# Kernel optimization log

Measured on AMD Instinct MI355X. Metric: run time of the kernel, lower is better.

The kernel has to match this reference:

```python
import jax, jax.numpy as jnp
import numpy as np

B, S, E = 16, 1024, 512
D = 2 * E            # dim of concatenated embeddings, input to QKV and MLP
H1, H2 = 2048, 1024  # hidden_dims
SCALE = float(1.0 / np.sqrt(E))  # code scales by embedding_dim**0.5 (the init arg, not D)


def setup_inputs() -> dict:
    key = jax.random.key(0)
    k = jax.random.split(key, 12)

    def lin_w(kk, fan_in, fan_out):
        return jax.random.normal(kk, (fan_in, fan_out), jnp.float32) * float(1.0 / np.sqrt(fan_in))

    return {
        "emb1": jax.random.normal(k[0], (B, S, E), jnp.float32),
        "emb2": jax.random.normal(k[1], (B, S, E), jnp.float32),
        # query-row masks; all ones (a 0 would -inf an entire softmax row -> NaN)
        "mask1": jnp.ones((B, S // 2), jnp.int32),
        "mask2": jnp.ones((B, S // 2), jnp.int32),
        "Wq": lin_w(k[2], D, D), "bq": jnp.zeros((D,), jnp.float32),
        "Wk": lin_w(k[3], D, D), "bk": jnp.zeros((D,), jnp.float32),
        "Wv": lin_w(k[4], D, D), "bv": jnp.zeros((D,), jnp.float32),
        "W1": lin_w(k[5], D, H1), "b1": jnp.zeros((H1,), jnp.float32),
        "W2": lin_w(k[6], H1, H2), "b2": jnp.zeros((H2,), jnp.float32),
        "W3": lin_w(k[7], H2, 1), "b3": jnp.zeros((1,), jnp.float32),
    }


def reference(emb1, emb2, mask1, mask2, Wq, bq, Wk, bk, Wv, bv, W1, b1, W2, b2, W3, b3):
    x = jnp.concatenate([emb1, emb2], axis=-1)        # [B, S, D]
    mask = jnp.concatenate([mask1, mask2], axis=-1)   # [B, S] (query-row mask)

    # QKV self-attention with query-only mask
    Q = x @ Wq + bq
    K = x @ Wk + bk
    V = x @ Wv + bv
    scores = jnp.einsum("bqd,bkd->bqk", Q, K) * SCALE  # [B, S, S]
    scores = jnp.where(mask[:, :, None] == 0, -jnp.inf, scores)
    attn = jax.nn.softmax(scores, axis=-1)
    attended = jnp.einsum("bqk,bkd->bqd", attn, V)     # [B, S, D]

    # MLP head (Dropout is identity in eval mode)
    h = jax.nn.relu(attended @ W1 + b1)
    h = jax.nn.relu(h @ W2 + b2)
    logits = h @ W3 + b3                               # [B, S, 1]
    return jax.nn.sigmoid(logits)
```

## Files before the change

### kernel.cpp

```cpp
#include <hip/hip_runtime.h>
#include <math.h>

#define DEV __device__ __forceinline__

typedef unsigned short u16;
typedef unsigned int   u32;
typedef __bf16 bf16x8 __attribute__((ext_vector_type(8)));
typedef float  f32x4  __attribute__((ext_vector_type(4)));
typedef u16    u16x8  __attribute__((ext_vector_type(8)));
typedef u16    u16x4  __attribute__((ext_vector_type(4)));

DEV u16 f2b(float f) {
  u32 u = __builtin_bit_cast(u32, f);
  u = (u + 0x7FFFu + ((u >> 16) & 1u)) >> 16;
  return (u16)u;
}
DEV float b2f(u16 h) { u32 u = (u32)h << 16; return __builtin_bit_cast(float, u); }

DEV void gl_lds16(const u16* g, u16* l) {
  __builtin_amdgcn_global_load_lds((const __attribute__((address_space(1))) void*)g,
                                   (__attribute__((address_space(3))) void*)l, 16, 0, 0);
}

DEV float wred_max(float v) {
#pragma unroll
  for (int o = 32; o > 0; o >>= 1) v = fmaxf(v, __shfl_xor(v, o, 64));
  return v;
}
DEV float wred_sum(float v) {
#pragma unroll
  for (int o = 32; o > 0; o >>= 1) v += __shfl_xor(v, o, 64);
  return v;
}

__global__ __launch_bounds__(256) void concat_convert(
    const float* __restrict__ e1, const float* __restrict__ e2, u16* __restrict__ xb) {
  const size_t idx = ((size_t)blockIdx.x * 256 + threadIdx.x) * 8;
  const int d = (int)(idx & 1023);
  const size_t row = idx >> 10;
  const float* s = (d < 512) ? (e1 + row * 512 + d) : (e2 + row * 512 + (d - 512));
  f32x4 a = *(const f32x4*)s;
  f32x4 b = *(const f32x4*)(s + 4);
  u16x8 o;
  o[0]=f2b(a[0]); o[1]=f2b(a[1]); o[2]=f2b(a[2]); o[3]=f2b(a[3]);
  o[4]=f2b(b[0]); o[5]=f2b(b[1]); o[6]=f2b(b[2]); o[7]=f2b(b[3]);
  *(u16x8*)(xb + idx) = o;
}

__global__ __launch_bounds__(256) void transpose_w(
    const float* __restrict__ W, int ldi, u16* __restrict__ WT, int ldo) {
  __shared__ float tile[64][65];
  const int tx = threadIdx.x & 63, ty = threadIdx.x >> 6;
  const int r0 = blockIdx.y * 64, c0 = blockIdx.x * 64;
#pragma unroll
  for (int i = 0; i < 16; ++i)
    tile[ty + 4*i][tx] = W[(size_t)(r0 + ty + 4*i) * ldi + c0 + tx];
  __syncthreads();
#pragma unroll
  for (int i = 0; i < 16; ++i)
    WT[(size_t)(c0 + ty + 4*i) * ldo + r0 + tx] = f2b(tile[tx][ty + 4*i]);
}

__global__ void concat_bias(const float* __restrict__ bq, const float* __restrict__ bk,
                            float* __restrict__ o) {
  int i = blockIdx.x * 256 + threadIdx.x;
  o[i] = (i < 1024) ? bq[i] : bk[i - 1024];
}

template<int F32OUT, int RELU, int RBIAS>
__global__ __launch_bounds__(512, 2) void gemm256(
    const u16* __restrict__ A, int lda, long long sA,
    const u16* __restrict__ B, int ldb, long long sB,
    void* __restrict__ C, int ldc, long long sC,
    const float* __restrict__ bias, float scale, int K) {
  __shared__ __align__(16) u16 lds[4][2][8192];

  const int t  = threadIdx.x;
  const int ln = t & 63, wv = t >> 6;

  int bx, by, bz;
  {
    const int gx = gridDim.x, gy = gridDim.y, gz = gridDim.z;
    const int nwg = gx * gy * gz;
    const int F = (blockIdx.z * gy + blockIdx.y) * gx + blockIdx.x;
    const int q = nwg >> 3;
    const int L = (F & 7) * q + (F >> 3);
    if (gz > 1) {
      const int pb = gx * gy;
      bz = L / pb; const int r = L - bz * pb;
      by = r / gx; bx = r - by * gx;
    } else {
      bz = 0;
      const int sh = ((gy & 7) == 0) ? 8 : 4;
      const int sw = gx * sh;
      const int sy = L / sw; const int r = L - sy * sw;
      bx = r / sh; by = sy * sh + (r - bx * sh);
    }
  }
  const int m0 = by * 256, n0 = bx * 256;
  A += (size_t)bz * (size_t)sA; B += (size_t)bz * (size_t)sB;

  const int srow = t >> 2;
  const int sgr  = (t & 3) ^ ((t >> 3) & 3);
  const u16* gA = A + (size_t)(m0 + srow) * lda + sgr * 8;
  const u16* gB = B + (size_t)(n0 + srow) * ldb + sgr * 8;
  const size_t a128 = (size_t)128 * lda, b128 = (size_t)128 * ldb;
  const int ldst = wv * 512;

  const int l15 = ln & 15, lhi = ln >> 4;
  const int wm = (wv >> 2) * 128, wn = (wv & 3) * 64;

  int offA[8], offB[4];
#pragma unroll
  for (int i = 0; i < 8; ++i) {
    const int r = wm + i * 16 + l15;
    offA[i] = r * 32 + ((lhi ^ ((r >> 1) & 3)) << 3);
  }
#pragma unroll
  for (int j = 0; j < 4; ++j) {
    const int r = wn + j * 16 + l15;
    offB[j] = r * 32 + ((lhi ^ ((r >> 1) & 3)) << 3);
  }

  f32x4 acc[8][4] = {};
  const int KT = K >> 5;

#pragma unroll
  for (int pt = 0; pt < 3; ++pt) {
    const u16* _ga = gA + (size_t)pt * 32;
    const u16* _gb = gB + (size_t)pt * 32;
    u16* _la = &lds[pt][0][ldst];
    u16* _lb = &lds[pt][1][ldst];
    gl_lds16(_ga, _la); gl_lds16(_ga + a128, _la + 4096);
    gl_lds16(_gb, _lb); gl_lds16(_gb + b128, _lb + 4096);
  }
  asm volatile("s_waitcnt vmcnt(8)" ::: "memory");
  __builtin_amdgcn_sched_barrier(0);
  __builtin_amdgcn_s_barrier();

  for (int kt = 0; kt < KT; ++kt) {
    const u16* Abuf = &lds[kt & 3][0][0];
    const u16* Bbuf = &lds[kt & 3][1][0];
    const int  nt   = kt + 3;

    bf16x8 a0 = *(const bf16x8*)&Abuf[offA[0]];
    bf16x8 a1 = *(const bf16x8*)&Abuf[offA[1]];
    bf16x8 a2 = *(const bf16x8*)&Abuf[offA[2]];
    bf16x8 a3 = *(const bf16x8*)&Abuf[offA[3]];
    bf16x8 b0 = *(const bf16x8*)&Bbuf[offB[0]];
    bf16x8 b1 = *(const bf16x8*)&Bbuf[offB[1]];
    bf16x8 b2 = *(const bf16x8*)&Bbuf[offB[2]];
    bf16x8 b3 = *(const bf16x8*)&Bbuf[offB[3]];
    if (nt < KT) {
      const u16* _ga = gA + (size_t)nt * 32;
      u16* _la = &lds[nt & 3][0][ldst];
      gl_lds16(_ga, _la); gl_lds16(_ga + a128, _la + 4096);
    }
    __builtin_amdgcn_s_barrier();
    __builtin_amdgcn_s_setprio(1);
    acc[0][0] = __builtin_amdgcn_mfma_f32_16x16x32_bf16(a0, b0, acc[0][0], 0, 0, 0);
    acc[0][1] = __builtin_amdgcn_mfma_f32_16x16x32_bf16(a0, b1, acc[0][1], 0, 0, 0);
    acc[0][2] = __builtin_amdgcn_mfma_f32_16x16x32_bf16(a0, b2, acc[0][2], 0, 0, 0);
    acc[0][3] = __builtin_amdgcn_mfma_f32_16x16x32_bf16(a0, b3, acc[0][3], 0, 0, 0);
    acc[1][0] = __builtin_amdgcn_mfma_f32_16x16x32_bf16(a1, b0, acc[1][0], 0, 0, 0);
    acc[1][1] = __builtin_amdgcn_mfma_f32_16x16x32_bf16(a1, b1, acc[1][1], 0, 0, 0);
    acc[1][2] = __builtin_amdgcn_mfma_f32_16x16x32_bf16(a1, b2, acc[1][2], 0, 0, 0);
    acc[1][3] = __builtin_amdgcn_mfma_f32_16x16x32_bf16(a1, b3, acc[1][3], 0, 0, 0);
    acc[2][0] = __builtin_amdgcn_mfma_f32_16x16x32_bf16(a2, b0, acc[2][0], 0, 0, 0);
    acc[2][1] = __builtin_amdgcn_mfma_f32_16x16x32_bf16(a2, b1, acc[2][1], 0, 0, 0);
    acc[2][2] = __builtin_amdgcn_mfma_f32_16x16x32_bf16(a2, b2, acc[2][2], 0, 0, 0);
    acc[2][3] = __builtin_amdgcn_mfma_f32_16x16x32_bf16(a2, b3, acc[2][3], 0, 0, 0);
    acc[3][0] = __builtin_amdgcn_mfma_f32_16x16x32_bf16(a3, b0, acc[3][0], 0, 0, 0);
    acc[3][1] = __builtin_amdgcn_mfma_f32_16x16x32_bf16(a3, b1, acc[3][1], 0, 0, 0);
    acc[3][2] = __builtin_amdgcn_mfma_f32_16x16x32_bf16(a3, b2, acc[3][2], 0, 0, 0);
    acc[3][3] = __builtin_amdgcn_mfma_f32_16x16x32_bf16(a3, b3, acc[3][3], 0, 0, 0);
    __builtin_amdgcn_s_setprio(0);
    __builtin_amdgcn_s_barrier();

    bf16x8 a4 = *(const bf16x8*)&Abuf[offA[4]];
    bf16x8 a5 = *(const bf16x8*)&Abuf[offA[5]];
    bf16x8 a6 = *(const bf16x8*)&Abuf[offA[6]];
    bf16x8 a7 = *(const bf16x8*)&Abuf[offA[7]];
    if (nt < KT) {
      const u16* _gb = gB + (size_t)nt * 32;
      u16* _lb = &lds[nt & 3][1][ldst];
      gl_lds16(_gb, _lb); gl_lds16(_gb + b128, _lb + 4096);
    }
    __builtin_amdgcn_s_barrier();
    __builtin_amdgcn_s_setprio(1);
    acc[4][0] = __builtin_amdgcn_mfma_f32_16x16x32_bf16(a4, b0, acc[4][0], 0, 0, 0);
    acc[4][1] = __builtin_amdgcn_mfma_f32_16x16x32_bf16(a4, b1, acc[4][1], 0, 0, 0);
    acc[4][2] = __builtin_amdgcn_mfma_f32_16x16x32_bf16(a4, b2, acc[4][2], 0, 0, 0);
    acc[4][3] = __builtin_amdgcn_mfma_f32_16x16x32_bf16(a4, b3, acc[4][3], 0, 0, 0);
    acc[5][0] = __builtin_amdgcn_mfma_f32_16x16x32_bf16(a5, b0, acc[5][0], 0, 0, 0);
    acc[5][1] = __builtin_amdgcn_mfma_f32_16x16x32_bf16(a5, b1, acc[5][1], 0, 0, 0);
    acc[5][2] = __builtin_amdgcn_mfma_f32_16x16x32_bf16(a5, b2, acc[5][2], 0, 0, 0);
    acc[5][3] = __builtin_amdgcn_mfma_f32_16x16x32_bf16(a5, b3, acc[5][3], 0, 0, 0);
    acc[6][0] = __builtin_amdgcn_mfma_f32_16x16x32_bf16(a6, b0, acc[6][0], 0, 0, 0);
    acc[6][1] = __builtin_amdgcn_mfma_f32_16x16x32_bf16(a6, b1, acc[6][1], 0, 0, 0);
    acc[6][2] = __builtin_amdgcn_mfma_f32_16x16x32_bf16(a6, b2, acc[6][2], 0, 0, 0);
    acc[6][3] = __builtin_amdgcn_mfma_f32_16x16x32_bf16(a6, b3, acc[6][3], 0, 0, 0);
    acc[7][0] = __builtin_amdgcn_mfma_f32_16x16x32_bf16(a7, b0, acc[7][0], 0, 0, 0);
    acc[7][1] = __builtin_amdgcn_mfma_f32_16x16x32_bf16(a7, b1, acc[7][1], 0, 0, 0);
    acc[7][2] = __builtin_amdgcn_mfma_f32_16x16x32_bf16(a7, b2, acc[7][2], 0, 0, 0);
    acc[7][3] = __builtin_amdgcn_mfma_f32_16x16x32_bf16(a7, b3, acc[7][3], 0, 0, 0);
    __builtin_amdgcn_s_setprio(0);

    if (kt < KT - 3)       { asm volatile("s_waitcnt vmcnt(8)" ::: "memory"); }
    else if (kt == KT - 3) { asm volatile("s_waitcnt vmcnt(4)" ::: "memory"); }
    else if (kt == KT - 2) { asm volatile("s_waitcnt vmcnt(0)" ::: "memory"); }
    __builtin_amdgcn_sched_barrier(0);
    __builtin_amdgcn_s_barrier();
  }

  const size_t cb = (size_t)bz * (size_t)sC;
#pragma unroll
  for (int i = 0; i < 8; ++i) {
    const int rg = m0 + wm + i * 16 + lhi * 4;
#pragma unroll
    for (int j = 0; j < 4; ++j) {
      const int cg = n0 + wn + j * 16 + l15;
      const float cbv = (!RBIAS && bias) ? bias[cg] : 0.f;
#pragma unroll
      for (int r = 0; r < 4; ++r) {
        float v = acc[i][j][r] * scale + (RBIAS ? bias[rg + r] : cbv);
        if (RELU) v = fmaxf(v, 0.f);
        if (F32OUT) ((float*)C)[cb + (size_t)(rg + r) * ldc + cg] = v;
        else        ((u16*)C)[cb + (size_t)(rg + r) * ldc + cg] = f2b(v);
      }
    }
  }
}

__global__ __launch_bounds__(256) void softmax_mask(
    const float* __restrict__ sc, const int* __restrict__ m1,
    const int* __restrict__ m2, u16* __restrict__ attn) {
  __shared__ float red[8];
  const int row = blockIdx.x;
  const int b = row >> 10, q = row & 1023;
  const int mk = (q < 512) ? m1[b * 512 + q] : m2[b * 512 + q - 512];
  f32x4 v = ((const f32x4*)(sc + (size_t)row * 1024))[threadIdx.x];
  if (mk == 0) { v[0] = v[1] = v[2] = v[3] = -INFINITY; }
  float mx = fmaxf(fmaxf(v[0], v[1]), fmaxf(v[2], v[3]));
  mx = wred_max(mx);
  const int ln = threadIdx.x & 63, wv = threadIdx.x >> 6;
  if (ln == 0) red[wv] = mx;
  __syncthreads();
  mx = fmaxf(fmaxf(red[0], red[1]), fmaxf(red[2], red[3]));
  float e0 = __expf(v[0] - mx), e1 = __expf(v[1] - mx);
  float e2 = __expf(v[2] - mx), e3 = __expf(v[3] - mx);
  float s = wred_sum(e0 + e1 + e2 + e3);
  if (ln == 0) red[4 + wv] = s;
  __syncthreads();
  const float inv = 1.f / (red[4] + red[5] + red[6] + red[7]);
  u16x4 o; o[0] = f2b(e0 * inv); o[1] = f2b(e1 * inv); o[2] = f2b(e2 * inv); o[3] = f2b(e3 * inv);
  *(u16x4*)(attn + (size_t)row * 1024 + threadIdx.x * 4) = o;
}

__global__ __launch_bounds__(256) void logits_sigmoid(
    const u16* __restrict__ h2, const float* __restrict__ W3,
    const float* __restrict__ b3, float* __restrict__ out) {
  const int wid = (blockIdx.x * 256 + threadIdx.x) >> 6;
  const int ln = threadIdx.x & 63;
  const u16* r = h2 + (size_t)wid * 1024 + ln * 16;
  u16x8 v0 = *(const u16x8*)r;
  u16x8 v1 = *(const u16x8*)(r + 8);
  const float* w = W3 + ln * 16;
  float s = 0.f;
#pragma unroll
  for (int i = 0; i < 8; ++i) s += b2f(v0[i]) * w[i];
#pragma unroll
  for (int i = 0; i < 8; ++i) s += b2f(v1[i]) * w[8 + i];
#pragma unroll
  for (int o = 32; o > 0; o >>= 1) s += __shfl_down(s, o, 64);
  if (ln == 0) out[wid] = 1.f / (1.f + __expf(-(s + b3[0])));
}

extern "C" void kernel_launch(void* const* d_in, const int* in_sizes, int n_in,
                              void* d_out, int out_size, void* d_ws, size_t ws_size,
                              hipStream_t stream) {
  (void)in_sizes; (void)n_in; (void)out_size; (void)ws_size;
  const float* emb1 = (const float*)d_in[0];
  const float* emb2 = (const float*)d_in[1];
  const int*   mask1 = (const int*)d_in[2];
  const int*   mask2 = (const int*)d_in[3];
  const float* Wq = (const float*)d_in[4];  const float* bq = (const float*)d_in[5];
  const float* Wk = (const float*)d_in[6];  const float* bk = (const float*)d_in[7];
  const float* Wv = (const float*)d_in[8];  const float* bv = (const float*)d_in[9];
  const float* W1 = (const float*)d_in[10]; const float* b1 = (const float*)d_in[11];
  const float* W2 = (const float*)d_in[12]; const float* b2 = (const float*)d_in[13];
  const float* W3 = (const float*)d_in[14]; const float* b3 = (const float*)d_in[15];

  char* ws = (char*)d_ws;
  u16*  XB    = (u16*)(ws + 0);
  u16*  QK    = (u16*)(ws + 33554432);
  u16*  VT    = (u16*)(ws + 100663296);
  float* SC   = (float*)(ws + 134217728);
  u16*  WTQKV = (u16*)(ws + 201326592);
  u16*  W1T   = (u16*)(ws + 207618048);
  u16*  W2T   = (u16*)(ws + 211812352);
  float* BF_  = (float*)(ws + 216006656);
  u16*  ATTN  = XB;
  u16*  ATT   = (u16*)(ws + 134217728);
  u16*  H1    = QK;
  u16*  H2    = VT;
  float* out  = (float*)d_out;

  const float SCALE = 0.04419417382415922f;

  concat_convert<<<8192, 256, 0, stream>>>(emb1, emb2, XB);
  transpose_w<<<dim3(16, 16), 256, 0, stream>>>(Wq, 1024, WTQKV, 1024);
  transpose_w<<<dim3(16, 16), 256, 0, stream>>>(Wk, 1024, WTQKV + 1024 * 1024, 1024);
  transpose_w<<<dim3(16, 16), 256, 0, stream>>>(Wv, 1024, WTQKV + 2048 * 1024, 1024);
  transpose_w<<<dim3(32, 16), 256, 0, stream>>>(W1, 2048, W1T, 1024);
  transpose_w<<<dim3(16, 32), 256, 0, stream>>>(W2, 1024, W2T, 2048);
  concat_bias<<<8, 256, 0, stream>>>(bq, bk, BF_);

  gemm256<0, 0, 0><<<dim3(8, 64, 1), 512, 0, stream>>>(
      XB, 1024, 0, WTQKV, 1024, 0, QK, 2048, 0, BF_, 1.f, 1024);
  gemm256<0, 0, 1><<<dim3(64, 4, 1), 512, 0, stream>>>(
      WTQKV + 2048 * 1024, 1024, 0, XB, 1024, 0, VT, 16384, 0, bv, 1.f, 1024);
  gemm256<1, 0, 0><<<dim3(4, 4, 16), 512, 0, stream>>>(
      QK, 2048, 2097152LL, QK + 1024, 2048, 2097152LL,
      SC, 1024, 1048576LL, nullptr, SCALE, 1024);
  softmax_mask<<<16384, 256, 0, stream>>>(SC, mask1, mask2, ATTN);
  gemm256<0, 0, 0><<<dim3(4, 4, 16), 512, 0, stream>>>(
      ATTN, 1024, 1048576LL, VT, 16384, 1024LL,
      ATT, 1024, 1048576LL, nullptr, 1.f, 1024);
  gemm256<0, 1, 0><<<dim3(8, 64, 1), 512, 0, stream>>>(
      ATT, 1024, 0, W1T, 1024, 0, H1, 2048, 0, b1, 1.f, 1024);
  gemm256<0, 1, 0><<<dim3(4, 64, 1), 512, 0, stream>>>(
      H1, 2048, 0, W2T, 2048, 0, H2, 1024, 0, b2, 1.f, 2048);
  logits_sigmoid<<<4096, 256, 0, stream>>>(H2, W3, b3, out);
}
```

Baseline: 414.0 us.

## Software-pipeline LDS fragment loads across k-iterations in the GEMM main loop

Restructures the GEMM k-loop so the A/B fragments for the next k-tile are read from LDS while the current tile's second-half MFMAs execute. Global-to-LDS staging for a tile is issued as a single block at the top of each iteration, and barriers drop from four to two per iteration, with manual lgkmcnt waits to order LDS reads against MFMAs. This aims to hide LDS read latency and barrier stalls behind matrix-core work. In exchange it raises register pressure from the extra live fragment registers, and the hand-set wait counts must match exactly for the kernel to stay correct.

```diff
diff --git a/kernel.cpp b/kernel.cpp
--- a/kernel.cpp
+++ b/kernel.cpp
@@ -2,6 +2,7 @@
 #include <math.h>
 
 #define DEV __device__ __forceinline__
+#define SB0() __builtin_amdgcn_sched_barrier(0)
 
 typedef unsigned short u16;
 typedef unsigned int   u32;
@@ -125,93 +126,91 @@
   f32x4 acc[8][4] = {};
   const int KT = K >> 5;
 
-#pragma unroll
-  for (int pt = 0; pt < 3; ++pt) {
-    const u16* _ga = gA + (size_t)pt * 32;
-    const u16* _gb = gB + (size_t)pt * 32;
-    u16* _la = &lds[pt][0][ldst];
-    u16* _lb = &lds[pt][1][ldst];
-    gl_lds16(_ga, _la); gl_lds16(_ga + a128, _la + 4096);
-    gl_lds16(_gb, _lb); gl_lds16(_gb + b128, _lb + 4096);
-  }
+#define STAGE(tile)                                                       \
+  {                                                                       \
+    const int rb = (tile) & 3;                                            \
+    const u16* _ga = gA + (size_t)(tile) * 32;                            \
+    const u16* _gb = gB + (size_t)(tile) * 32;                            \
+    u16* _la = &lds[rb][0][ldst];                                         \
+    u16* _lb = &lds[rb][1][ldst];                                         \
+    gl_lds16(_ga, _la); gl_lds16(_ga + a128, _la + 4096);                 \
+    gl_lds16(_gb, _lb); gl_lds16(_gb + b128, _lb + 4096);                 \
+  }
+#define MF(i, j, Av, Bv) \
+  acc[i][j] = __builtin_amdgcn_mfma_f32_16x16x32_bf16(Av, Bv, acc[i][j], 0, 0, 0)
+
+  STAGE(0); STAGE(1); STAGE(2);
   asm volatile("s_waitcnt vmcnt(8)" ::: "memory");
-  __builtin_amdgcn_sched_barrier(0);
+  SB0();
   __builtin_amdgcn_s_barrier();
+  bf16x8 pa0, pa1, pa2, pa3, pb0, pb1, pb2, pb3;
+  {
+    const u16* Ab = &lds[0][0][0];
+    const u16* Bb = &lds[0][1][0];
+    pb0 = *(const bf16x8*)&Bb[offB[0]]; pb1 = *(const bf16x8*)&Bb[offB[1]];
+    pb2 = *(const bf16x8*)&Bb[offB[2]]; pb3 = *(const bf16x8*)&Bb[offB[3]];
+    pa0 = *(const bf16x8*)&Ab[offA[0]]; pa1 = *(const bf16x8*)&Ab[offA[1]];
+    pa2 = *(const bf16x8*)&Ab[offA[2]]; pa3 = *(const bf16x8*)&Ab[offA[3]];
+  }
 
   for (int kt = 0; kt < KT; ++kt) {
-    const u16* Abuf = &lds[kt & 3][0][0];
-    const u16* Bbuf = &lds[kt & 3][1][0];
-    const int  nt   = kt + 3;
-
-    bf16x8 a0 = *(const bf16x8*)&Abuf[offA[0]];
-    bf16x8 a1 = *(const bf16x8*)&Abuf[offA[1]];
-    bf16x8 a2 = *(const bf16x8*)&Abuf[offA[2]];
-    bf16x8 a3 = *(const bf16x8*)&Abuf[offA[3]];
-    bf16x8 b0 = *(const bf16x8*)&Bbuf[offB[0]];
-    bf16x8 b1 = *(const bf16x8*)&Bbuf[offB[1]];
-    bf16x8 b2 = *(const bf16x8*)&Bbuf[offB[2]];
-    bf16x8 b3 = *(const bf16x8*)&Bbuf[offB[3]];
-    if (nt < KT) {
-      const u16* _ga = gA + (size_t)nt * 32;
-      u16* _la = &lds[nt & 3][0][ldst];
-      gl_lds16(_ga, _la); gl_lds16(_ga + a128, _la + 4096);
-    }
-    __builtin_amdgcn_s_barrier();
-    __builtin_amdgcn_s_setprio(1);
-    acc[0][0] = __builtin_amdgcn_mfma_f32_16x16x32_bf16(a0, b0, acc[0][0], 0, 0, 0);
-    acc[0][1] = __builtin_amdgcn_mfma_f32_16x16x32_bf16(a0, b1, acc[0][1], 0, 0, 0);
-    acc[0][2] = __builtin_amdgcn_mfma_f32_16x16x32_bf16(a0, b2, acc[0][2], 0, 0, 0);
-    acc[0][3] = __builtin_amdgcn_mfma_f32_16x16x32_bf16(a0, b3, acc[0][3], 0, 0, 0);
-    acc[1][0] = __builtin_amdgcn_mfma_f32_16x16x32_bf16(a1, b0, acc[1][0], 0, 0, 0);
-    acc[1][1] = __builtin_amdgcn_mfma_f32_16x16x32_bf16(a1, b1, acc[1][1], 0, 0, 0);
-    acc[1][2] = __builtin_amdgcn_mfma_f32_16x16x32_bf16(a1, b2, acc[1][2], 0, 0, 0);
-    acc[1][3] = __builtin_amdgcn_mfma_f32_16x16x32_bf16(a1, b3, acc[1][3], 0, 0, 0);
-    acc[2][0] = __builtin_amdgcn_mfma_f32_16x16x32_bf16(a2, b0, acc[2][0], 0, 0, 0);
-    acc[2][1] = __builtin_amdgcn_mfma_f32_16x16x32_bf16(a2, b1, acc[2][1], 0, 0, 0);
-    acc[2][2] = __builtin_amdgcn_mfma_f32_16x16x32_bf16(a2, b2, acc[2][2], 0, 0, 0);
-    acc[2][3] = __builtin_amdgcn_mfma_f32_16x16x32_bf16(a2, b3, acc[2][3], 0, 0, 0);
-    acc[3][0] = __builtin_amdgcn_mfma_f32_16x16x32_bf16(a3, b0, acc[3][0], 0, 0, 0);
-    acc[3][1] = __builtin_amdgcn_mfma_f32_16x16x32_bf16(a3, b1, acc[3][1], 0, 0, 0);
-    acc[3][2] = __builtin_amdgcn_mfma_f32_16x16x32_bf16(a3, b2, acc[3][2], 0, 0, 0);
-    acc[3][3] = __builtin_amdgcn_mfma_f32_16x16x32_bf16(a3, b3, acc[3][3], 0, 0, 0);
-    __builtin_amdgcn_s_setprio(0);
-    __builtin_amdgcn_s_barrier();
-
-    bf16x8 a4 = *(const bf16x8*)&Abuf[offA[4]];
-    bf16x8 a5 = *(const bf16x8*)&Abuf[offA[5]];
-    bf16x8 a6 = *(const bf16x8*)&Abuf[offA[6]];
-    bf16x8 a7 = *(const bf16x8*)&Abuf[offA[7]];
-    if (nt < KT) {
-      const u16* _gb = gB + (size_t)nt * 32;
-      u16* _lb = &lds[nt & 3][1][ldst];
-      gl_lds16(_gb, _lb); gl_lds16(_gb + b128, _lb + 4096);
-    }
-    __builtin_amdgcn_s_barrier();
-    __builtin_amdgcn_s_setprio(1);
-    acc[4][0] = __builtin_amdgcn_mfma_f32_16x16x32_bf16(a4, b0, acc[4][0], 0, 0, 0);
-    acc[4][1] = __builtin_amdgcn_mfma_f32_16x16x32_bf16(a4, b1, acc[4][1], 0, 0, 0);
-    acc[4][2] = __builtin_amdgcn_mfma_f32_16x16x32_bf16(a4, b2, acc[4][2], 0, 0, 0);
-    acc[4][3] = __builtin_amdgcn_mfma_f32_16x16x32_bf16(a4, b3, acc[4][3], 0, 0, 0);
-    acc[5][0] = __builtin_amdgcn_mfma_f32_16x16x32_bf16(a5, b0, acc[5][0], 0, 0, 0);
-    acc[5][1] = __builtin_amdgcn_mfma_f32_16x16x32_bf16(a5, b1, acc[5][1], 0, 0, 0);
-    acc[5][2] = __builtin_amdgcn_mfma_f32_16x16x32_bf16(a5, b2, acc[5][2], 0, 0, 0);
-    acc[5][3] = __builtin_amdgcn_mfma_f32_16x16x32_bf16(a5, b3, acc[5][3], 0, 0, 0);
-    acc[6][0] = __builtin_amdgcn_mfma_f32_16x16x32_bf16(a6, b0, acc[6][0], 0, 0, 0);
-    acc[6][1] = __builtin_amdgcn_mfma_f32_16x16x32_bf16(a6, b1, acc[6][1], 0, 0, 0);
-    acc[6][2] = __builtin_amdgcn_mfma_f32_16x16x32_bf16(a6, b2, acc[6][2], 0, 0, 0);
-    acc[6][3] = __builtin_amdgcn_mfma_f32_16x16x32_bf16(a6, b3, acc[6][3], 0, 0, 0);
-    acc[7][0] = __builtin_amdgcn_mfma_f32_16x16x32_bf16(a7, b0, acc[7][0], 0, 0, 0);
-    acc[7][1] = __builtin_amdgcn_mfma_f32_16x16x32_bf16(a7, b1, acc[7][1], 0, 0, 0);
-    acc[7][2] = __builtin_amdgcn_mfma_f32_16x16x32_bf16(a7, b2, acc[7][2], 0, 0, 0);
-    acc[7][3] = __builtin_amdgcn_mfma_f32_16x16x32_bf16(a7, b3, acc[7][3], 0, 0, 0);
-    __builtin_amdgcn_s_setprio(0);
-
+    const u16* Ab = &lds[kt & 3][0][0];
+
+    if (kt + 3 < KT) STAGE(kt + 3);
+    bf16x8 a4 = *(const bf16x8*)&Ab[offA[4]];
+    bf16x8 a5 = *(const bf16x8*)&Ab[offA[5]];
+    bf16x8 a6 = *(const bf16x8*)&Ab[offA[6]];
+    bf16x8 a7 = *(const bf16x8*)&Ab[offA[7]];
     if (kt < KT - 3)       { asm volatile("s_waitcnt vmcnt(8)" ::: "memory"); }
     else if (kt == KT - 3) { asm volatile("s_waitcnt vmcnt(4)" ::: "memory"); }
     else if (kt == KT - 2) { asm volatile("s_waitcnt vmcnt(0)" ::: "memory"); }
-    __builtin_amdgcn_sched_barrier(0);
+    SB0();
     __builtin_amdgcn_s_barrier();
-  }
+    asm volatile("s_waitcnt lgkmcnt(4)" ::: "memory");
+    SB0();
+    __builtin_amdgcn_s_setprio(1);
+    MF(0,0,pa0,pb0); MF(0,1,pa0,pb1); MF(0,2,pa0,pb2); MF(0,3,pa0,pb3);
+    MF(1,0,pa1,pb0); MF(1,1,pa1,pb1); MF(1,2,pa1,pb2); MF(1,3,pa1,pb3);
+    MF(2,0,pa2,pb0); MF(2,1,pa2,pb1); MF(2,2,pa2,pb2); MF(2,3,pa2,pb3);
+    MF(3,0,pa3,pb0); MF(3,1,pa3,pb1); MF(3,2,pa3,pb2); MF(3,3,pa3,pb3);
+    __builtin_amdgcn_s_setprio(0);
+
+    if (kt + 1 < KT) {
+      const u16* Ab2 = &lds[(kt + 1) & 3][0][0];
+      const u16* Bb2 = &lds[(kt + 1) & 3][1][0];
+      bf16x8 nb0 = *(const bf16x8*)&Bb2[offB[0]];
+      bf16x8 nb1 = *(const bf16x8*)&Bb2[offB[1]];
+      bf16x8 nb2 = *(const bf16x8*)&Bb2[offB[2]];
+      bf16x8 nb3 = *(const bf16x8*)&Bb2[offB[3]];
+      bf16x8 na0 = *(const bf16x8*)&Ab2[offA[0]];
+      bf16x8 na1 = *(const bf16x8*)&Ab2[offA[1]];
+      bf16x8 na2 = *(const bf16x8*)&Ab2[offA[2]];
+      bf16x8 na3 = *(const bf16x8*)&Ab2[offA[3]];
+      asm volatile("s_waitcnt lgkmcnt(8)" ::: "memory");
+      SB0();
+      __builtin_amdgcn_s_setprio(1);
+      MF(4,0,a4,pb0); MF(4,1,a4,pb1); MF(4,2,a4,pb2); MF(4,3,a4,pb3);
+      MF(5,0,a5,pb0); MF(5,1,a5,pb1); MF(5,2,a5,pb2); MF(5,3,a5,pb3);
+      MF(6,0,a6,pb0); MF(6,1,a6,pb1); MF(6,2,a6,pb2); MF(6,3,a6,pb3);
+      MF(7,0,a7,pb0); MF(7,1,a7,pb1); MF(7,2,a7,pb2); MF(7,3,a7,pb3);
+      __builtin_amdgcn_s_setprio(0);
+      pa0 = na0; pa1 = na1; pa2 = na2; pa3 = na3;
+      pb0 = nb0; pb1 = nb1; pb2 = nb2; pb3 = nb3;
+    } else {
+      asm volatile("s_waitcnt lgkmcnt(0)" ::: "memory");
+      SB0();
+      __builtin_amdgcn_s_setprio(1);
+      MF(4,0,a4,pb0); MF(4,1,a4,pb1); MF(4,2,a4,pb2); MF(4,3,a4,pb3);
+      MF(5,0,a5,pb0); MF(5,1,a5,pb1); MF(5,2,a5,pb2); MF(5,3,a5,pb3);
+      MF(6,0,a6,pb0); MF(6,1,a6,pb1); MF(6,2,a6,pb2); MF(6,3,a6,pb3);
+      MF(7,0,a7,pb0); MF(7,1,a7,pb1); MF(7,2,a7,pb2); MF(7,3,a7,pb3);
+      __builtin_amdgcn_s_setprio(0);
+    }
+    SB0();
+    __builtin_amdgcn_s_barrier();
+  }
+#undef MF
+#undef STAGE
 
   const size_t cb = (size_t)bz * (size_t)sC;
 #pragma unroll
```

Result: no change. 416.5 us (+0.6%).
